# Optimization experiments

Measured on AMD Instinct MI355X. Metric: run time of the kernel, lower is better.

The kernel has to match this reference:

```python
import jax, jax.numpy as jnp
import numpy as np

NUM_USERS = 100000
NUM_ITEMS = 50000
N_NODES = NUM_USERS + NUM_ITEMS
D = 64
N_LAYERS = 3
E = 2000000
B = 1024
ALPHA_PREF = 1.0


def setup_inputs() -> dict:
    key = jax.random.key(0)
    k1, k2, k3, k4 = jax.random.split(key, 4)
    embed = jax.random.normal(k1, (N_NODES, D), dtype=jnp.float32) * 0.1
    edge_index = jax.random.randint(k2, (2, E), 0, N_NODES, dtype=jnp.int32)
    users = jax.random.randint(k3, (B,), 0, NUM_USERS, dtype=jnp.int32)
    items = jax.random.randint(k4, (B,), 0, NUM_ITEMS, dtype=jnp.int32)
    return {"embed": embed, "edge_index": edge_index, "users": users, "items": items}


def _lightgcn_propagate(x, row, col, norm):
    # message: norm * x[row] (x_j = source), aggregated (add) at col (target)
    msg = norm[:, None] * x[row]                      # [E, D]
    return jnp.zeros_like(x).at[col].add(msg)         # [N, D]


def reference(embed, edge_index, users, items):
    row, col = edge_index[0], edge_index[1]
    n = embed.shape[0]
    # degree normalization (depends only on edge_index; same every layer)
    deg = jnp.zeros((n,), jnp.float32).at[row].add(1.0)
    deg_inv = jnp.clip(deg, 1.0, None) ** -0.5
    norm = deg_inv[row] * deg_inv[col]                # [E]

    x = embed
    for _ in range(N_LAYERS):
        x = _lightgcn_propagate(x, row, col, norm)

    u_emb = x[users]                                  # [B, D]
    i_emb = x[items + NUM_USERS]                      # [B, D]

    # mask = (row == users[:,None]) flattened selection of col; edge e is
    # selected once per batch element b with users[b] == row[e] -> multiplicity
    cnt = jnp.zeros((n,), jnp.float32).at[users].add(1.0)
    mult = cnt[row]                                   # [E] selection multiplicity

    # PreferenceShapley surrogate: softmax over selected neighbor embeddings
    # of alpha_pref * <neigh_emb, mean(u_emb)>, flattened over the batch.
    context = u_emb.mean(0)                           # [D]
    neigh = x[col]                                    # [E, D]
    logits = ALPHA_PREF * (neigh @ context)           # [E]
    masked = jnp.where(mult > 0, logits, -jnp.inf)
    mx = jnp.max(masked)
    ew = mult * jnp.exp(logits - mx)                  # [E] weighted exp (0 where unselected)
    z = jnp.clip(ew.sum(), 1e-12, None)
    neigh_aggr = (ew[:, None] * neigh).sum(0) / z     # [D]

    score = (u_emb * i_emb).sum(-1) + u_emb @ neigh_aggr  # [B]
    return jax.nn.sigmoid(score)
```

## Files before the change

### kernel.cpp

```cpp
#include <hip/hip_runtime.h>
#include <float.h>
#include <math.h>

#define NUM_USERS 100000
#define NUM_ITEMS 50000
#define NNODES    150000
#define DIM       64
#define NEDGE     2000000
#define BATCH     1024
#define SEL_CAP   (1 << 18)
#define LOGIT_BLOCKS 512

#define SLICES   1024
#define EPS      1956
#define NBUK     293

__device__ __forceinline__ float wave_sum64(float v) {
    #pragma unroll
    for (int off = 32; off > 0; off >>= 1) v += __shfl_xor(v, off, 64);
    return v;
}

__device__ __forceinline__ float bf2f(unsigned short s) {
    return __uint_as_float(((unsigned int)s) << 16);
}
__device__ __forceinline__ unsigned short f2bf(float f) {
    unsigned int u = __float_as_uint(f);
    return (unsigned short)((u + 0x7fffu + ((u >> 16) & 1u)) >> 16);
}


__global__ __launch_bounds__(512) void bhist_kernel(
        const int* __restrict__ row, const int* __restrict__ col,
        const int* __restrict__ ucnt,
        unsigned short* __restrict__ cntR, unsigned short* __restrict__ cntC,
        unsigned char* __restrict__ rkR, unsigned char* __restrict__ rkC,
        int* __restrict__ n_sel, int* __restrict__ sel_col, float* __restrict__ sel_w) {
    __shared__ unsigned int hr[NBUK], hc[NBUK];
    __shared__ int lcnt, lbase;
    __shared__ int2 buf[256];
    int blk = blockIdx.x, t = threadIdx.x;
    for (int i = t; i < NBUK; i += 512) { hr[i] = 0; hc[i] = 0; }
    if (t == 0) lcnt = 0;
    __syncthreads();
    int e0 = blk * EPS;
    int e1 = e0 + EPS; if (e1 > NEDGE) e1 = NEDGE;
    for (int base = e0 + t * 4; base < e1; base += 2048) {
        if (base + 4 <= e1) {
            int4 r4 = *(const int4*)(row + base);
            int4 c4 = *(const int4*)(col + base);
            uchar4 a, b;
            a.x = (unsigned char)atomicAdd(&hr[r4.x >> 9], 1u);
            a.y = (unsigned char)atomicAdd(&hr[r4.y >> 9], 1u);
            a.z = (unsigned char)atomicAdd(&hr[r4.z >> 9], 1u);
            a.w = (unsigned char)atomicAdd(&hr[r4.w >> 9], 1u);
            b.x = (unsigned char)atomicAdd(&hc[c4.x >> 9], 1u);
            b.y = (unsigned char)atomicAdd(&hc[c4.y >> 9], 1u);
            b.z = (unsigned char)atomicAdd(&hc[c4.z >> 9], 1u);
            b.w = (unsigned char)atomicAdd(&hc[c4.w >> 9], 1u);
            *(uchar4*)(rkR + base) = a;
            *(uchar4*)(rkC + base) = b;
            int u0 = ucnt[r4.x], u1 = ucnt[r4.y], u2 = ucnt[r4.z], u3 = ucnt[r4.w];
            if (u0 > 0) { int i = atomicAdd(&lcnt, 1); if (i < 256) buf[i] = make_int2(c4.x, u0); }
            if (u1 > 0) { int i = atomicAdd(&lcnt, 1); if (i < 256) buf[i] = make_int2(c4.y, u1); }
            if (u2 > 0) { int i = atomicAdd(&lcnt, 1); if (i < 256) buf[i] = make_int2(c4.z, u2); }
            if (u3 > 0) { int i = atomicAdd(&lcnt, 1); if (i < 256) buf[i] = make_int2(c4.w, u3); }
        } else {
            for (int e = base; e < e1; ++e) {
                int r = row[e], c = col[e];
                rkR[e] = (unsigned char)atomicAdd(&hr[r >> 9], 1u);
                rkC[e] = (unsigned char)atomicAdd(&hc[c >> 9], 1u);
                int u = ucnt[r];
                if (u > 0) { int i = atomicAdd(&lcnt, 1); if (i < 256) buf[i] = make_int2(c, u); }
            }
        }
    }
    __syncthreads();
    for (int i = t; i < NBUK; i += 512) {
        cntR[(size_t)blk * NBUK + i] = (unsigned short)hr[i];
        cntC[(size_t)blk * NBUK + i] = (unsigned short)hc[i];
    }
    if (t == 0) {
        int c = lcnt; c = c < 256 ? c : 256;
        lbase = atomicAdd(n_sel, c);
    }
    __syncthreads();
    int c = lcnt; c = c < 256 ? c : 256;
    int b = lbase;
    for (int i = t; i < c; i += 512) {
        int o = b + i;
        if (o < SEL_CAP) { sel_col[o] = buf[i].x; sel_w[o] = (float)buf[i].y; }
    }
}


__global__ __launch_bounds__(512) void bprefix1_kernel(
        const unsigned short* __restrict__ cntR, const unsigned short* __restrict__ cntC,
        unsigned short* __restrict__ offR, unsigned short* __restrict__ offC,
        int* __restrict__ totRC) {
    int side = blockIdx.x / NBUK;
    int b = blockIdx.x - side * NBUK;
    const unsigned short* cnt = side ? cntC : cntR;
    unsigned short* off = side ? offC : offR;
    __shared__ int sm[512];
    int t = threadIdx.x;
    int v0 = (int)cnt[(size_t)(2 * t) * NBUK + b];
    int v1 = (int)cnt[(size_t)(2 * t + 1) * NBUK + b];
    int p = v0 + v1;
    sm[t] = p;
    __syncthreads();
    for (int o = 1; o < 512; o <<= 1) {
        int x = (t >= o) ? sm[t - o] : 0;
        __syncthreads();
        sm[t] += x;
        __syncthreads();
    }
    int excl = sm[t] - p;
    off[(size_t)(2 * t) * NBUK + b]     = (unsigned short)excl;
    off[(size_t)(2 * t + 1) * NBUK + b] = (unsigned short)(excl + v0);
    if (t == 511) totRC[side * NBUK + b] = sm[511];
}

__global__ __launch_bounds__(512) void bprefix2_kernel(
        const int* __restrict__ totRC, int* __restrict__ baseR, int* __restrict__ baseC) {
    const int* tot = totRC + blockIdx.x * NBUK;
    int* base = blockIdx.x ? baseC : baseR;
    __shared__ int sm[512];
    int t = threadIdx.x;
    int v = (t < NBUK) ? tot[t] : 0;
    sm[t] = v;
    __syncthreads();
    for (int o = 1; o < 512; o <<= 1) {
        int x = (t >= o) ? sm[t - o] : 0;
        __syncthreads();
        sm[t] += x;
        __syncthreads();
    }
    if (t < NBUK) base[t] = sm[t] - v;
    if (t == NBUK - 1) base[NBUK] = sm[t];
}


__global__ __launch_bounds__(512) void place_kernel(
        const int* __restrict__ row, const int* __restrict__ col,
        const unsigned char* __restrict__ rkR, const unsigned char* __restrict__ rkC,
        const unsigned short* __restrict__ cntR, const unsigned short* __restrict__ cntC,
        const unsigned short* __restrict__ offR, const unsigned short* __restrict__ offC,
        const int* __restrict__ baseR, const int* __restrict__ baseC,
        unsigned short* __restrict__ midR, unsigned int* __restrict__ midC) {
    __shared__ int lofC[NBUK], lofR[NBUK], posC[NBUK], posR[NBUK];
    __shared__ int cCl[NBUK], cRl[NBUK];
    __shared__ int scan_tmp[512];
    __shared__ unsigned int   stC[EPS];
    __shared__ unsigned short stR[EPS];
    __shared__ unsigned short bmapC[EPS], bmapR[EPS];
    int blk = blockIdx.x, t = threadIdx.x;
    if (t < NBUK) {
        cCl[t] = (int)cntC[(size_t)blk * NBUK + t];
        cRl[t] = (int)cntR[(size_t)blk * NBUK + t];
        posC[t] = baseC[t] + (int)offC[(size_t)blk * NBUK + t];
        posR[t] = baseR[t] + (int)offR[(size_t)blk * NBUK + t];
    }
    __syncthreads();
    scan_tmp[t] = (t < NBUK) ? cCl[t] : 0;
    __syncthreads();
    for (int o = 1; o < 512; o <<= 1) {
        int v = (t >= o) ? scan_tmp[t - o] : 0;
        __syncthreads();
        scan_tmp[t] += v;
        __syncthreads();
    }
    if (t < NBUK) lofC[t] = scan_tmp[t] - cCl[t];
    __syncthreads();
    scan_tmp[t] = (t < NBUK) ? cRl[t] : 0;
    __syncthreads();
    for (int o = 1; o < 512; o <<= 1) {
        int v = (t >= o) ? scan_tmp[t - o] : 0;
        __syncthreads();
        scan_tmp[t] += v;
        __syncthreads();
    }
    if (t < NBUK) lofR[t] = scan_tmp[t] - cRl[t];
    __syncthreads();
    if (t < NBUK) {
        int c = cCl[t], lo = lofC[t];
        for (int k = 0; k < c; ++k) bmapC[lo + k] = (unsigned short)t;
        c = cRl[t]; lo = lofR[t];
        for (int k = 0; k < c; ++k) bmapR[lo + k] = (unsigned short)t;
    }
    int e0 = blk * EPS;
    int e1 = e0 + EPS; if (e1 > NEDGE) e1 = NEDGE;
    for (int base = e0 + t * 4; base < e1; base += 2048) {
        if (base + 4 <= e1) {
            int4 r4 = *(const int4*)(row + base);
            int4 c4 = *(const int4*)(col + base);
            uchar4 kr = *(const uchar4*)(rkR + base);
            uchar4 kc = *(const uchar4*)(rkC + base);
            stC[lofC[c4.x >> 9] + (int)kc.x] = ((unsigned int)(c4.x & 511) << 18) | (unsigned int)r4.x;
            stC[lofC[c4.y >> 9] + (int)kc.y] = ((unsigned int)(c4.y & 511) << 18) | (unsigned int)r4.y;
            stC[lofC[c4.z >> 9] + (int)kc.z] = ((unsigned int)(c4.z & 511) << 18) | (unsigned int)r4.z;
            stC[lofC[c4.w >> 9] + (int)kc.w] = ((unsigned int)(c4.w & 511) << 18) | (unsigned int)r4.w;
            stR[lofR[r4.x >> 9] + (int)kr.x] = (unsigned short)(r4.x & 511);
            stR[lofR[r4.y >> 9] + (int)kr.y] = (unsigned short)(r4.y & 511);
            stR[lofR[r4.z >> 9] + (int)kr.z] = (unsigned short)(r4.z & 511);
            stR[lofR[r4.w >> 9] + (int)kr.w] = (unsigned short)(r4.w & 511);
        } else {
            for (int e = base; e < e1; ++e) {
                int r = row[e], c = col[e];
                stC[lofC[c >> 9] + (int)rkC[e]] = ((unsigned int)(c & 511) << 18) | (unsigned int)r;
                stR[lofR[r >> 9] + (int)rkR[e]] = (unsigned short)(r & 511);
            }
        }
    }
    __syncthreads();
    int total = e1 - e0;
    for (int j = t; j < total; j += 512) {
        int b = bmapC[j];
        midC[posC[b] + (j - lofC[b])] = stC[j];
        b = bmapR[j];
        midR[posR[b] + (j - lofR[b])] = stR[j];
    }
}


__global__ __launch_bounds__(1024) void bfinal_kernel(
        const unsigned int* __restrict__ midC, const int* __restrict__ baseC,
        const unsigned short* __restrict__ midR, const int* __restrict__ baseR,
        const float4* __restrict__ embed,
        int* __restrict__ rptr, int* __restrict__ src_sorted,
        float* __restrict__ dinv, float* __restrict__ dinv2,
        uint2* __restrict__ y0) {
    __shared__ int cnt[512], sm[512], cur[512];
    __shared__ float dinvL[512];
    int b = blockIdx.x, t = threadIdx.x;
    int s0 = baseC[b], s1 = baseC[b + 1];
    if (t < 512) cnt[t] = 0;
    __syncthreads();
    for (int i = s0 + t; i < s1; i += 1024) atomicAdd(&cnt[midC[i] >> 18], 1);
    __syncthreads();
    if (t < 512) sm[t] = cnt[t];
    __syncthreads();
    for (int off = 1; off < 512; off <<= 1) {
        int v = 0;
        if (t < 512 && t >= off) v = sm[t - off];
        __syncthreads();
        if (t < 512) sm[t] += v;
        __syncthreads();
    }
    if (t < 512) {
        int excl = s0 + sm[t] - cnt[t];
        int n = b * 512 + t;
        if (n < NNODES) rptr[n] = excl;
        cur[t] = excl;
    }
    if (b == NBUK - 1 && t == 0) rptr[NNODES] = s1;
    if (b == 0 && t < 16) y0[(size_t)NNODES * 16 + t] = make_uint2(0u, 0u);
    __syncthreads();
    for (int i = s0 + t; i < s1; i += 1024) {
        unsigned int v = midC[i];
        int dst = atomicAdd(&cur[v >> 18], 1);
        src_sorted[dst] = (int)(v & 0x3FFFFu);
    }
    __syncthreads();
    if (t < 512) cnt[t] = 0;
    __syncthreads();
    int r0 = baseR[b], r1 = baseR[b + 1];
    for (int i = r0 + t; i < r1; i += 1024) atomicAdd(&cnt[midR[i]], 1);
    __syncthreads();
    if (t < 512) {
        int n = b * 512 + t;
        if (n < NNODES) {
            float d = fmaxf((float)cnt[t], 1.0f);
            float di = rsqrtf(d);
            dinv[n] = di; dinv2[n] = 1.0f / d;
            dinvL[t] = di;
        }
    }
    __syncthreads();
    int nbase = b * 512;
    int nmax = NNODES - nbase; if (nmax > 512) nmax = 512;
    if (nmax < 0) nmax = 0;
    for (int i = t; i < nmax * 16; i += 1024) {
        int ln = i >> 4, slot = i & 15;
        float d = dinvL[ln];
        float4 v = embed[(size_t)(nbase + ln) * 16 + slot];
        unsigned int w0 = (unsigned int)f2bf(v.x * d) | ((unsigned int)f2bf(v.y * d) << 16);
        unsigned int w1 = (unsigned int)f2bf(v.z * d) | ((unsigned int)f2bf(v.w * d) << 16);
        y0[(size_t)(nbase + ln) * 16 + slot] = make_uint2(w0, w1);
    }
}


#define ACC8(V) do { \
    a0 += __uint_as_float((V).x << 16); a1 += __uint_as_float((V).x & 0xffff0000u); \
    a2 += __uint_as_float((V).y << 16); a3 += __uint_as_float((V).y & 0xffff0000u); \
    a4 += __uint_as_float((V).z << 16); a5 += __uint_as_float((V).z & 0xffff0000u); \
    a6 += __uint_as_float((V).w << 16); a7 += __uint_as_float((V).w & 0xffff0000u); \
} while (0)

__device__ __forceinline__ void prop_node(
        const uint4* __restrict__ x_in, uint4* __restrict__ x_out,
        const int* __restrict__ ptr, const int* __restrict__ src,
        const float* __restrict__ scale, int node, int sl) {
    int i = ptr[node], e = ptr[node + 1];
    float sc = scale[node];
    float a0 = 0.f, a1 = 0.f, a2 = 0.f, a3 = 0.f;
    float a4 = 0.f, a5 = 0.f, a6 = 0.f, a7 = 0.f;
    int p0, p1, p2, p3;
    if (i + 4 <= e) { p0 = src[i]; p1 = src[i + 1]; p2 = src[i + 2]; p3 = src[i + 3]; }
    while (i + 8 <= e) {
        uint4 w0 = x_in[p0 * 8 + sl];
        uint4 w1 = x_in[p1 * 8 + sl];
        uint4 w2 = x_in[p2 * 8 + sl];
        uint4 w3 = x_in[p3 * 8 + sl];
        p0 = src[i + 4]; p1 = src[i + 5]; p2 = src[i + 6]; p3 = src[i + 7];
        i += 4;
        ACC8(w0); ACC8(w1); ACC8(w2); ACC8(w3);
    }
    if (i + 4 <= e) {
        uint4 w0 = x_in[p0 * 8 + sl];
        uint4 w1 = x_in[p1 * 8 + sl];
        uint4 w2 = x_in[p2 * 8 + sl];
        uint4 w3 = x_in[p3 * 8 + sl];
        i += 4;
        ACC8(w0); ACC8(w1); ACC8(w2); ACC8(w3);
    }
    if (i < e) {
        int q0 = src[i];
        int q1 = (i + 1 < e) ? src[i + 1] : NNODES;
        int q2 = (i + 2 < e) ? src[i + 2] : NNODES;
        uint4 w0 = x_in[q0 * 8 + sl];
        uint4 w1 = x_in[q1 * 8 + sl];
        uint4 w2 = x_in[q2 * 8 + sl];
        ACC8(w0); ACC8(w1); ACC8(w2);
    }
    uint4 o;
    o.x = (unsigned int)f2bf(a0 * sc) | ((unsigned int)f2bf(a1 * sc) << 16);
    o.y = (unsigned int)f2bf(a2 * sc) | ((unsigned int)f2bf(a3 * sc) << 16);
    o.z = (unsigned int)f2bf(a4 * sc) | ((unsigned int)f2bf(a5 * sc) << 16);
    o.w = (unsigned int)f2bf(a6 * sc) | ((unsigned int)f2bf(a7 * sc) << 16);
    x_out[(size_t)node * 8 + sl] = o;
}

__global__ __launch_bounds__(256, 8) void prop_kernel(
        const uint4* __restrict__ x_in, uint4* __restrict__ x_out,
        const int* __restrict__ ptr, const int* __restrict__ src,
        const float* __restrict__ scale) {
    int gid  = blockIdx.x * blockDim.x + threadIdx.x;
    int node = gid >> 3;
    int sl   = gid & 7;
    if (node > NNODES) return;
    if (node == NNODES) {
        x_out[(size_t)node * 8 + sl] = make_uint4(0u, 0u, 0u, 0u);
        return;
    }
    prop_node(x_in, x_out, ptr, src, scale, node, sl);
}

__global__ __launch_bounds__(256, 8) void prop_list_kernel(
        const uint4* __restrict__ x_in, uint4* __restrict__ x_out,
        const int* __restrict__ ptr, const int* __restrict__ src,
        const float* __restrict__ scale,
        const int* __restrict__ users, const int* __restrict__ items,
        const int* __restrict__ sel_col, const int* __restrict__ n_sel_p) {
    int gid = blockIdx.x * blockDim.x + threadIdx.x;
    int li  = gid >> 3;
    int sl  = gid & 7;
    int node;
    if (li < BATCH) {
        node = users[li];
    } else if (li < 2 * BATCH) {
        node = items[li - BATCH] + NUM_USERS;
    } else {
        int j = li - 2 * BATCH;
        int n = *n_sel_p; if (n > SEL_CAP) n = SEL_CAP;
        if (j >= n) return;
        node = sel_col[j];
    }
    prop_node(x_in, x_out, ptr, src, scale, node, sl);
}


__global__ void ucnt_kernel(const int* __restrict__ users, int* __restrict__ ucnt) {
    int b = blockIdx.x * blockDim.x + threadIdx.x;
    if (b < BATCH) atomicAdd(&ucnt[users[b]], 1);
}

__global__ __launch_bounds__(256) void ctx_part_kernel(
        const unsigned short* __restrict__ x, const int* __restrict__ users,
        float* __restrict__ partial) {
    __shared__ float sm[256];
    int lane = threadIdx.x & 63, wl = threadIdx.x >> 6;
    int b = blockIdx.x * 4 + wl;
    float v = (b < BATCH) ? bf2f(x[users[b] * DIM + lane]) : 0.0f;
    sm[threadIdx.x] = v;
    __syncthreads();
    if (wl == 0)
        partial[blockIdx.x * 64 + lane] =
            sm[lane] + sm[64 + lane] + sm[128 + lane] + sm[192 + lane];
}

__global__ __launch_bounds__(256) void ctx_reduce_kernel(
        const float* __restrict__ partial, float* __restrict__ ctx) {
    __shared__ float sm[256];
    int lane = threadIdx.x & 63, wl = threadIdx.x >> 6;
    float acc = 0.0f;
    for (int i = wl; i < 256; i += 4) acc += partial[i * 64 + lane];
    sm[threadIdx.x] = acc;
    __syncthreads();
    if (wl == 0)
        ctx[lane] = (sm[lane] + sm[64 + lane] + sm[128 + lane] + sm[192 + lane])
                    * (1.0f / BATCH);
}

__global__ void softmax_kernel(const unsigned short* __restrict__ x,
                               const float* __restrict__ ctx,
                               const int* __restrict__ sel_col,
                               const float* __restrict__ sel_w,
                               const int* __restrict__ n_sel_p,
                               float* __restrict__ S, float* __restrict__ zp) {
    __shared__ float smS[4 * 64];
    __shared__ float smZ[4];
    int lane = threadIdx.x & 63, wl = threadIdx.x >> 6;
    int n = *n_sel_p; if (n > SEL_CAP) n = SEL_CAP;
    float c = ctx[lane];
    float accS = 0.0f, accZ = 0.0f;
    int stride = gridDim.x * 4;
    for (int idx = blockIdx.x * 4 + wl; idx < n; idx += stride) {
        int node = sel_col[idx];
        float xv = bf2f(x[node * DIM + lane]);
        float v = wave_sum64(xv * c);
        float w = sel_w[idx] * __expf(v);
        accS = fmaf(w, xv, accS);
        accZ += w;
    }
    smS[wl * 64 + lane] = accS;
    if (lane == 0) smZ[wl] = accZ;
    __syncthreads();
    if (wl == 0) {
        float s = smS[lane] + smS[64 + lane] + smS[128 + lane] + smS[192 + lane];
        atomicAdd(&S[lane], s);
    }
    if (threadIdx.x == 0) atomicAdd(zp, smZ[0] + smZ[1] + smZ[2] + smZ[3]);
}

__global__ void score_kernel(const unsigned short* __restrict__ x, const int* __restrict__ users,
                             const int* __restrict__ items, const float* __restrict__ S,
                             const float* __restrict__ zp, float* __restrict__ out) {
    int gid = blockIdx.x * blockDim.x + threadIdx.x;
    int b = gid >> 6, lane = gid & 63;
    if (b >= BATCH) return;
    float z = fmaxf(*zp, 1e-12f);
    float na = S[lane] / z;
    int u = users[b], it = items[b] + NUM_USERS;
    float v = bf2f(x[u * DIM + lane]) * (bf2f(x[it * DIM + lane]) + na);
    v = wave_sum64(v);
    if (lane == 0) out[b] = 1.0f / (1.0f + __expf(-v));
}


extern "C" void kernel_launch(void* const* d_in, const int* in_sizes, int n_in,
                              void* d_out, int out_size, void* d_ws, size_t ws_size,
                              hipStream_t stream) {
    const float* embed = (const float*)d_in[0];
    const int*   edge  = (const int*)d_in[1];
    const int*   row   = edge;
    const int*   col   = edge + NEDGE;
    const int*   users = (const int*)d_in[2];
    const int*   items = (const int*)d_in[3];
    float*       out   = (float*)d_out;
    char*        ws    = (char*)d_ws;

    size_t off = 0;
    auto A = [&](size_t bytes) { size_t o = off; off += (bytes + 255) & ~(size_t)255; return o; };
    size_t o_mid   = A((size_t)NEDGE * 4 + (size_t)NEDGE * 2);
    size_t o_xa    = A((size_t)(NNODES + 1) * DIM * 2);
    size_t o_xb    = A((size_t)(NNODES + 1) * DIM * 2);
    size_t o_src   = A((size_t)NEDGE * 4);
    size_t o_rkR   = A((size_t)SLICES * EPS);
    size_t o_rkC   = A((size_t)SLICES * EPS);
    size_t o_cntR  = A((size_t)SLICES * NBUK * 2);
    size_t o_cntC  = A((size_t)SLICES * NBUK * 2);
    size_t o_offR  = A((size_t)SLICES * NBUK * 2);
    size_t o_offC  = A((size_t)SLICES * NBUK * 2);
    size_t o_tot   = A((size_t)2 * NBUK * 4);
    size_t o_baseR = A((size_t)(NBUK + 1) * 4);
    size_t o_baseC = A((size_t)(NBUK + 1) * 4);
    size_t o_selc  = A((size_t)SEL_CAP * 4);
    size_t o_selw  = A((size_t)SEL_CAP * 4);
    size_t o_part  = A((size_t)256 * 64 * 4);
    size_t o_zero  = off;
    size_t o_ucnt  = A((size_t)NNODES * 4);
    size_t o_misc  = A(1024);
    size_t zero_bytes = off - o_zero;
    size_t o_dinv  = A((size_t)NNODES * 4);
    size_t o_dinv2 = A((size_t)NNODES * 4);
    size_t o_rptr  = A((size_t)(NNODES + 1) * 4);
    size_t o_ctx   = A(256);

    unsigned int*   midC = (unsigned int*)(ws + o_mid);
    unsigned short* midR = (unsigned short*)(ws + o_mid + (size_t)NEDGE * 4);
    unsigned short* xa   = (unsigned short*)(ws + o_xa);
    unsigned short* xb   = (unsigned short*)(ws + o_xb);
    int*   srcS  = (int*)(ws + o_src);
    unsigned char* rkR = (unsigned char*)(ws + o_rkR);
    unsigned char* rkC = (unsigned char*)(ws + o_rkC);
    unsigned short* cntR = (unsigned short*)(ws + o_cntR);
    unsigned short* cntC = (unsigned short*)(ws + o_cntC);
    unsigned short* offR = (unsigned short*)(ws + o_offR);
    unsigned short* offC = (unsigned short*)(ws + o_offC);
    int*   totRC = (int*)(ws + o_tot);
    int*   baseR = (int*)(ws + o_baseR);
    int*   baseC = (int*)(ws + o_baseC);
    int*   selc  = (int*)(ws + o_selc);
    float* selw  = (float*)(ws + o_selw);
    float* part  = (float*)(ws + o_part);
    int*   ucnt  = (int*)(ws + o_ucnt);
    int*   nsel  = (int*)(ws + o_misc);
    float* zp    = (float*)(ws + o_misc + 8);
    float* S     = (float*)(ws + o_misc + 256);
    float* dinv  = (float*)(ws + o_dinv);
    float* dinv2 = (float*)(ws + o_dinv2);
    int*   rptr  = (int*)(ws + o_rptr);
    float* ctx   = (float*)(ws + o_ctx);

    hipMemsetAsync(ws + o_zero, 0, zero_bytes, stream);

    ucnt_kernel<<<(BATCH + 255) / 256, 256, 0, stream>>>(users, ucnt);

    bhist_kernel<<<SLICES, 512, 0, stream>>>(row, col, ucnt, cntR, cntC, rkR, rkC,
                                             nsel, selc, selw);
    bprefix1_kernel<<<2 * NBUK, 512, 0, stream>>>(cntR, cntC, offR, offC, totRC);
    bprefix2_kernel<<<2, 512, 0, stream>>>(totRC, baseR, baseC);
    place_kernel<<<SLICES, 512, 0, stream>>>(row, col, rkR, rkC, cntR, cntC,
                                             offR, offC, baseR, baseC, midR, midC);
    bfinal_kernel<<<NBUK, 1024, 0, stream>>>(midC, baseC, midR, baseR,
                                             (const float4*)embed, rptr, srcS,
                                             dinv, dinv2, (uint2*)xa);

    int prop_blocks = ((NNODES + 1) * 8 + 255) / 256;
    prop_kernel<<<prop_blocks, 256, 0, stream>>>((const uint4*)xa, (uint4*)xb, rptr, srcS, dinv2);
    prop_kernel<<<prop_blocks, 256, 0, stream>>>((const uint4*)xb, (uint4*)xa, rptr, srcS, dinv2);
    int list_blocks = ((2 * BATCH + SEL_CAP) * 8 + 255) / 256;
    prop_list_kernel<<<list_blocks, 256, 0, stream>>>((const uint4*)xa, (uint4*)xb,
                                                      rptr, srcS, dinv,
                                                      users, items, selc, nsel);

    ctx_part_kernel<<<256, 256, 0, stream>>>(xb, users, part);
    ctx_reduce_kernel<<<1, 256, 0, stream>>>(part, ctx);
    softmax_kernel<<<LOGIT_BLOCKS, 256, 0, stream>>>(xb, ctx, selc, selw, nsel, S, zp);

    score_kernel<<<(BATCH * 64 + 255) / 256, 256, 0, stream>>>(xb, users, items, S, zp, out);
}
```

Before: 279.8 us.

## Recompute scatter ranks in place kernel, grid-stride list prop, fuse ctx reduction

The per-edge rank bytes are no longer written out by the histogram kernel and read back by the place kernel. The place kernel now recomputes each edge's in-bucket rank with its own shared-memory atomics, which removes about 4 MB of global round-trip traffic. Separately, the list propagation kernel now runs on a fixed 1024-block grid-stride launch instead of launching for the worst-case capacity. The two-kernel context reduction is merged into one kernel that adds into a zeroed buffer with global atomics. Recomputed ranks may not match the histogram order, but only the within-bucket order within a slice changes, and float atomics make the context sum order nondeterministic.

Result: faster. 262.7 us (-6.1%).

```diff
diff --git a/kernel.cpp b/kernel.cpp
--- a/kernel.cpp
+++ b/kernel.cpp
@@ -34,7 +34,6 @@
         const int* __restrict__ row, const int* __restrict__ col,
         const int* __restrict__ ucnt,
         unsigned short* __restrict__ cntR, unsigned short* __restrict__ cntC,
-        unsigned char* __restrict__ rkR, unsigned char* __restrict__ rkC,
         int* __restrict__ n_sel, int* __restrict__ sel_col, float* __restrict__ sel_w) {
     __shared__ unsigned int hr[NBUK], hc[NBUK];
     __shared__ int lcnt, lbase;
@@ -49,17 +48,14 @@
         if (base + 4 <= e1) {
             int4 r4 = *(const int4*)(row + base);
             int4 c4 = *(const int4*)(col + base);
-            uchar4 a, b;
-            a.x = (unsigned char)atomicAdd(&hr[r4.x >> 9], 1u);
-            a.y = (unsigned char)atomicAdd(&hr[r4.y >> 9], 1u);
-            a.z = (unsigned char)atomicAdd(&hr[r4.z >> 9], 1u);
-            a.w = (unsigned char)atomicAdd(&hr[r4.w >> 9], 1u);
-            b.x = (unsigned char)atomicAdd(&hc[c4.x >> 9], 1u);
-            b.y = (unsigned char)atomicAdd(&hc[c4.y >> 9], 1u);
-            b.z = (unsigned char)atomicAdd(&hc[c4.z >> 9], 1u);
-            b.w = (unsigned char)atomicAdd(&hc[c4.w >> 9], 1u);
-            *(uchar4*)(rkR + base) = a;
-            *(uchar4*)(rkC + base) = b;
+            atomicAdd(&hr[r4.x >> 9], 1u);
+            atomicAdd(&hr[r4.y >> 9], 1u);
+            atomicAdd(&hr[r4.z >> 9], 1u);
+            atomicAdd(&hr[r4.w >> 9], 1u);
+            atomicAdd(&hc[c4.x >> 9], 1u);
+            atomicAdd(&hc[c4.y >> 9], 1u);
+            atomicAdd(&hc[c4.z >> 9], 1u);
+            atomicAdd(&hc[c4.w >> 9], 1u);
             int u0 = ucnt[r4.x], u1 = ucnt[r4.y], u2 = ucnt[r4.z], u3 = ucnt[r4.w];
             if (u0 > 0) { int i = atomicAdd(&lcnt, 1); if (i < 256) buf[i] = make_int2(c4.x, u0); }
             if (u1 > 0) { int i = atomicAdd(&lcnt, 1); if (i < 256) buf[i] = make_int2(c4.y, u1); }
@@ -68,8 +64,8 @@
         } else {
             for (int e = base; e < e1; ++e) {
                 int r = row[e], c = col[e];
-                rkR[e] = (unsigned char)atomicAdd(&hr[r >> 9], 1u);
-                rkC[e] = (unsigned char)atomicAdd(&hc[c >> 9], 1u);
+                atomicAdd(&hr[r >> 9], 1u);
+                atomicAdd(&hc[c >> 9], 1u);
                 int u = ucnt[r];
                 if (u > 0) { int i = atomicAdd(&lcnt, 1); if (i < 256) buf[i] = make_int2(c, u); }
             }
@@ -143,13 +139,13 @@
 
 __global__ __launch_bounds__(512) void place_kernel(
         const int* __restrict__ row, const int* __restrict__ col,
-        const unsigned char* __restrict__ rkR, const unsigned char* __restrict__ rkC,
         const unsigned short* __restrict__ cntR, const unsigned short* __restrict__ cntC,
         const unsigned short* __restrict__ offR, const unsigned short* __restrict__ offC,
         const int* __restrict__ baseR, const int* __restrict__ baseC,
         unsigned short* __restrict__ midR, unsigned int* __restrict__ midC) {
     __shared__ int lofC[NBUK], lofR[NBUK], posC[NBUK], posR[NBUK];
     __shared__ int cCl[NBUK], cRl[NBUK];
+    __shared__ unsigned int hrP[NBUK], hcP[NBUK];
     __shared__ int scan_tmp[512];
     __shared__ unsigned int   stC[EPS];
     __shared__ unsigned short stR[EPS];
@@ -188,27 +184,37 @@
         c = cRl[t]; lo = lofR[t];
         for (int k = 0; k < c; ++k) bmapR[lo + k] = (unsigned short)t;
     }
+    for (int i = t; i < NBUK; i += 512) { hrP[i] = 0; hcP[i] = 0; }
+    __syncthreads();
     int e0 = blk * EPS;
     int e1 = e0 + EPS; if (e1 > NEDGE) e1 = NEDGE;
     for (int base = e0 + t * 4; base < e1; base += 2048) {
         if (base + 4 <= e1) {
             int4 r4 = *(const int4*)(row + base);
             int4 c4 = *(const int4*)(col + base);
-            uchar4 kr = *(const uchar4*)(rkR + base);
-            uchar4 kc = *(const uchar4*)(rkC + base);
-            stC[lofC[c4.x >> 9] + (int)kc.x] = ((unsigned int)(c4.x & 511) << 18) | (unsigned int)r4.x;
-            stC[lofC[c4.y >> 9] + (int)kc.y] = ((unsigned int)(c4.y & 511) << 18) | (unsigned int)r4.y;
-            stC[lofC[c4.z >> 9] + (int)kc.z] = ((unsigned int)(c4.z & 511) << 18) | (unsigned int)r4.z;
-            stC[lofC[c4.w >> 9] + (int)kc.w] = ((unsigned int)(c4.w & 511) << 18) | (unsigned int)r4.w;
-            stR[lofR[r4.x >> 9] + (int)kr.x] = (unsigned short)(r4.x & 511);
-            stR[lofR[r4.y >> 9] + (int)kr.y] = (unsigned short)(r4.y & 511);
-            stR[lofR[r4.z >> 9] + (int)kr.z] = (unsigned short)(r4.z & 511);
-            stR[lofR[r4.w >> 9] + (int)kr.w] = (unsigned short)(r4.w & 511);
+            unsigned int kc0 = atomicAdd(&hcP[c4.x >> 9], 1u);
+            unsigned int kc1 = atomicAdd(&hcP[c4.y >> 9], 1u);
+            unsigned int kc2 = atomicAdd(&hcP[c4.z >> 9], 1u);
+            unsigned int kc3 = atomicAdd(&hcP[c4.w >> 9], 1u);
+            stC[lofC[c4.x >> 9] + (int)kc0] = ((unsigned int)(c4.x & 511) << 18) | (unsigned int)r4.x;
+            stC[lofC[c4.y >> 9] + (int)kc1] = ((unsigned int)(c4.y & 511) << 18) | (unsigned int)r4.y;
+            stC[lofC[c4.z >> 9] + (int)kc2] = ((unsigned int)(c4.z & 511) << 18) | (unsigned int)r4.z;
+            stC[lofC[c4.w >> 9] + (int)kc3] = ((unsigned int)(c4.w & 511) << 18) | (unsigned int)r4.w;
+            unsigned int kr0 = atomicAdd(&hrP[r4.x >> 9], 1u);
+            unsigned int kr1 = atomicAdd(&hrP[r4.y >> 9], 1u);
+            unsigned int kr2 = atomicAdd(&hrP[r4.z >> 9], 1u);
+            unsigned int kr3 = atomicAdd(&hrP[r4.w >> 9], 1u);
+            stR[lofR[r4.x >> 9] + (int)kr0] = (unsigned short)(r4.x & 511);
+            stR[lofR[r4.y >> 9] + (int)kr1] = (unsigned short)(r4.y & 511);
+            stR[lofR[r4.z >> 9] + (int)kr2] = (unsigned short)(r4.z & 511);
+            stR[lofR[r4.w >> 9] + (int)kr3] = (unsigned short)(r4.w & 511);
         } else {
             for (int e = base; e < e1; ++e) {
                 int r = row[e], c = col[e];
-                stC[lofC[c >> 9] + (int)rkC[e]] = ((unsigned int)(c & 511) << 18) | (unsigned int)r;
-                stR[lofR[r >> 9] + (int)rkR[e]] = (unsigned short)(r & 511);
+                unsigned int kc = atomicAdd(&hcP[c >> 9], 1u);
+                stC[lofC[c >> 9] + (int)kc] = ((unsigned int)(c & 511) << 18) | (unsigned int)r;
+                unsigned int kr = atomicAdd(&hrP[r >> 9], 1u);
+                stR[lofR[r >> 9] + (int)kr] = (unsigned short)(r & 511);
             }
         }
     }
@@ -363,21 +369,22 @@
         const float* __restrict__ scale,
         const int* __restrict__ users, const int* __restrict__ items,
         const int* __restrict__ sel_col, const int* __restrict__ n_sel_p) {
-    int gid = blockIdx.x * blockDim.x + threadIdx.x;
-    int li  = gid >> 3;
-    int sl  = gid & 7;
-    int node;
-    if (li < BATCH) {
-        node = users[li];
-    } else if (li < 2 * BATCH) {
-        node = items[li - BATCH] + NUM_USERS;
-    } else {
-        int j = li - 2 * BATCH;
-        int n = *n_sel_p; if (n > SEL_CAP) n = SEL_CAP;
-        if (j >= n) return;
-        node = sel_col[j];
-    }
-    prop_node(x_in, x_out, ptr, src, scale, node, sl);
+    int n = *n_sel_p; if (n > SEL_CAP) n = SEL_CAP;
+    int total = (2 * BATCH + n) * 8;
+    int nth = gridDim.x * blockDim.x;
+    for (int gid = blockIdx.x * blockDim.x + threadIdx.x; gid < total; gid += nth) {
+        int li = gid >> 3;
+        int sl = gid & 7;
+        int node;
+        if (li < BATCH) {
+            node = users[li];
+        } else if (li < 2 * BATCH) {
+            node = items[li - BATCH] + NUM_USERS;
+        } else {
+            node = sel_col[li - 2 * BATCH];
+        }
+        prop_node(x_in, x_out, ptr, src, scale, node, sl);
+    }
 }
 
 
@@ -388,29 +395,18 @@
 
 __global__ __launch_bounds__(256) void ctx_part_kernel(
         const unsigned short* __restrict__ x, const int* __restrict__ users,
-        float* __restrict__ partial) {
+        float* __restrict__ ctx) {
     __shared__ float sm[256];
     int lane = threadIdx.x & 63, wl = threadIdx.x >> 6;
-    int b = blockIdx.x * 4 + wl;
-    float v = (b < BATCH) ? bf2f(x[users[b] * DIM + lane]) : 0.0f;
-    sm[threadIdx.x] = v;
+    int b0 = blockIdx.x * 16 + wl * 4;
+    float acc = 0.0f;
+    #pragma unroll
+    for (int k = 0; k < 4; ++k)
+        acc += bf2f(x[users[b0 + k] * DIM + lane]);
+    sm[threadIdx.x] = acc;
     __syncthreads();
     if (wl == 0)
-        partial[blockIdx.x * 64 + lane] =
-            sm[lane] + sm[64 + lane] + sm[128 + lane] + sm[192 + lane];
-}
-
-__global__ __launch_bounds__(256) void ctx_reduce_kernel(
-        const float* __restrict__ partial, float* __restrict__ ctx) {
-    __shared__ float sm[256];
-    int lane = threadIdx.x & 63, wl = threadIdx.x >> 6;
-    float acc = 0.0f;
-    for (int i = wl; i < 256; i += 4) acc += partial[i * 64 + lane];
-    sm[threadIdx.x] = acc;
-    __syncthreads();
-    if (wl == 0)
-        ctx[lane] = (sm[lane] + sm[64 + lane] + sm[128 + lane] + sm[192 + lane])
-                    * (1.0f / BATCH);
+        atomicAdd(&ctx[lane], sm[lane] + sm[64 + lane] + sm[128 + lane] + sm[192 + lane]);
 }
 
 __global__ void softmax_kernel(const unsigned short* __restrict__ x,
@@ -423,7 +419,7 @@
     __shared__ float smZ[4];
     int lane = threadIdx.x & 63, wl = threadIdx.x >> 6;
     int n = *n_sel_p; if (n > SEL_CAP) n = SEL_CAP;
-    float c = ctx[lane];
+    float c = ctx[lane] * (1.0f / BATCH);
     float accS = 0.0f, accZ = 0.0f;
     int stride = gridDim.x * 4;
     for (int idx = blockIdx.x * 4 + wl; idx < n; idx += stride) {
@@ -477,8 +473,6 @@
     size_t o_xa    = A((size_t)(NNODES + 1) * DIM * 2);
     size_t o_xb    = A((size_t)(NNODES + 1) * DIM * 2);
     size_t o_src   = A((size_t)NEDGE * 4);
-    size_t o_rkR   = A((size_t)SLICES * EPS);
-    size_t o_rkC   = A((size_t)SLICES * EPS);
     size_t o_cntR  = A((size_t)SLICES * NBUK * 2);
     size_t o_cntC  = A((size_t)SLICES * NBUK * 2);
     size_t o_offR  = A((size_t)SLICES * NBUK * 2);
@@ -488,7 +482,6 @@
     size_t o_baseC = A((size_t)(NBUK + 1) * 4);
     size_t o_selc  = A((size_t)SEL_CAP * 4);
     size_t o_selw  = A((size_t)SEL_CAP * 4);
-    size_t o_part  = A((size_t)256 * 64 * 4);
     size_t o_zero  = off;
     size_t o_ucnt  = A((size_t)NNODES * 4);
     size_t o_misc  = A(1024);
@@ -496,15 +489,12 @@
     size_t o_dinv  = A((size_t)NNODES * 4);
     size_t o_dinv2 = A((size_t)NNODES * 4);
     size_t o_rptr  = A((size_t)(NNODES + 1) * 4);
-    size_t o_ctx   = A(256);
 
     unsigned int*   midC = (unsigned int*)(ws + o_mid);
     unsigned short* midR = (unsigned short*)(ws + o_mid + (size_t)NEDGE * 4);
     unsigned short* xa   = (unsigned short*)(ws + o_xa);
     unsigned short* xb   = (unsigned short*)(ws + o_xb);
     int*   srcS  = (int*)(ws + o_src);
-    unsigned char* rkR = (unsigned char*)(ws + o_rkR);
-    unsigned char* rkC = (unsigned char*)(ws + o_rkC);
     unsigned short* cntR = (unsigned short*)(ws + o_cntR);
     unsigned short* cntC = (unsigned short*)(ws + o_cntC);
     unsigned short* offR = (unsigned short*)(ws + o_offR);
@@ -514,25 +504,24 @@
     int*   baseC = (int*)(ws + o_baseC);
     int*   selc  = (int*)(ws + o_selc);
     float* selw  = (float*)(ws + o_selw);
-    float* part  = (float*)(ws + o_part);
     int*   ucnt  = (int*)(ws + o_ucnt);
     int*   nsel  = (int*)(ws + o_misc);
     float* zp    = (float*)(ws + o_misc + 8);
     float* S     = (float*)(ws + o_misc + 256);
+    float* ctx   = (float*)(ws + o_misc + 512);
     float* dinv  = (float*)(ws + o_dinv);
     float* dinv2 = (float*)(ws + o_dinv2);
     int*   rptr  = (int*)(ws + o_rptr);
-    float* ctx   = (float*)(ws + o_ctx);
 
     hipMemsetAsync(ws + o_zero, 0, zero_bytes, stream);
 
     ucnt_kernel<<<(BATCH + 255) / 256, 256, 0, stream>>>(users, ucnt);
 
-    bhist_kernel<<<SLICES, 512, 0, stream>>>(row, col, ucnt, cntR, cntC, rkR, rkC,
+    bhist_kernel<<<SLICES, 512, 0, stream>>>(row, col, ucnt, cntR, cntC,
                                              nsel, selc, selw);
     bprefix1_kernel<<<2 * NBUK, 512, 0, stream>>>(cntR, cntC, offR, offC, totRC);
     bprefix2_kernel<<<2, 512, 0, stream>>>(totRC, baseR, baseC);
-    place_kernel<<<SLICES, 512, 0, stream>>>(row, col, rkR, rkC, cntR, cntC,
+    place_kernel<<<SLICES, 512, 0, stream>>>(row, col, cntR, cntC,
                                              offR, offC, baseR, baseC, midR, midC);
     bfinal_kernel<<<NBUK, 1024, 0, stream>>>(midC, baseC, midR, baseR,
                                              (const float4*)embed, rptr, srcS,
@@ -541,13 +530,11 @@
     int prop_blocks = ((NNODES + 1) * 8 + 255) / 256;
     prop_kernel<<<prop_blocks, 256, 0, stream>>>((const uint4*)xa, (uint4*)xb, rptr, srcS, dinv2);
     prop_kernel<<<prop_blocks, 256, 0, stream>>>((const uint4*)xb, (uint4*)xa, rptr, srcS, dinv2);
-    int list_blocks = ((2 * BATCH + SEL_CAP) * 8 + 255) / 256;
-    prop_list_kernel<<<list_blocks, 256, 0, stream>>>((const uint4*)xa, (uint4*)xb,
-                                                      rptr, srcS, dinv,
-                                                      users, items, selc, nsel);
-
-    ctx_part_kernel<<<256, 256, 0, stream>>>(xb, users, part);
-    ctx_reduce_kernel<<<1, 256, 0, stream>>>(part, ctx);
+    prop_list_kernel<<<1024, 256, 0, stream>>>((const uint4*)xa, (uint4*)xb,
+                                               rptr, srcS, dinv,
+                                               users, items, selc, nsel);
+
+    ctx_part_kernel<<<64, 256, 0, stream>>>(xb, users, ctx);
     softmax_kernel<<<LOGIT_BLOCKS, 256, 0, stream>>>(xb, ctx, selc, selw, nsel, S, zp);
 
     score_kernel<<<(BATCH * 64 + 255) / 256, 256, 0, stream>>>(xb, users, items, S, zp, out);
```
